# Kernel optimization log

Hardware: AMD Instinct MI355X
Metric: run time of the kernel (lower is better)

Reference implementation:

```python
import jax, jax.numpy as jnp
import numpy as np

D_MODEL = 1024
NUM_HEADS = 16
LN_EPS = 1e-5


def setup_inputs() -> dict:
    key = jax.random.key(0)
    ks = jax.random.split(key, 8)
    d = D_MODEL
    x = jax.random.normal(ks[0], (8, 1024, d), dtype=jnp.float32)
    # nn.MultiheadAttention parameters (combined in_proj, out_proj)
    in_proj_w = jax.random.normal(ks[1], (3 * d, d), dtype=jnp.float32) / np.sqrt(d)
    in_proj_b = jnp.zeros((3 * d,), dtype=jnp.float32)
    out_proj_w = jax.random.normal(ks[2], (d, d), dtype=jnp.float32) / np.sqrt(d)
    out_proj_b = jnp.zeros((d,), dtype=jnp.float32)
    ln_w = jnp.ones((d,), dtype=jnp.float32)
    ln_b = jnp.zeros((d,), dtype=jnp.float32)
    time_decay = jnp.asarray(0.1, dtype=jnp.float32)
    return {"x": x, "time_decay": time_decay, "in_proj_w": in_proj_w,
            "in_proj_b": in_proj_b, "out_proj_w": out_proj_w,
            "out_proj_b": out_proj_b, "ln_w": ln_w, "ln_b": ln_b}


def reference(x, time_decay, in_proj_w, in_proj_b, out_proj_w, out_proj_b, ln_w, ln_b):
    B, S, d = x.shape
    H = NUM_HEADS
    hd = d // H
    # vectorized time-decay bias: -|time_decay| * |i - j|  (replaces nested loop)
    idx = jnp.arange(S, dtype=jnp.float32)
    attn_bias = -jnp.abs(time_decay) * jnp.abs(idx[:, None] - idx[None, :])  # [S,S]
    # combined QKV projection
    qkv = x @ in_proj_w.T + in_proj_b  # [B,S,3d]
    q, k, v = jnp.split(qkv, 3, axis=-1)
    q = q.reshape(B, S, H, hd)
    k = k.reshape(B, S, H, hd)
    v = v.reshape(B, S, H, hd)
    scale = 1.0 / np.sqrt(hd)
    scores = jnp.einsum('bqhd,bkhd->bhqk', q, k) * scale + attn_bias  # [B,H,S,S]
    weights = jax.nn.softmax(scores, axis=-1)
    attn = jnp.einsum('bhqk,bkhd->bqhd', weights, v).reshape(B, S, d)
    attn_out = attn @ out_proj_w.T + out_proj_b
    # need_weights=True with default average_attn_weights=True -> mean over heads
    attn_weights = jnp.mean(weights, axis=1)  # [B,S,S]
    # residual + LayerNorm
    y = x + attn_out
    mu = jnp.mean(y, axis=-1, keepdims=True)
    var = jnp.mean(jnp.square(y - mu), axis=-1, keepdims=True)
    out = (y - mu) / jnp.sqrt(var + LN_EPS) * ln_w + ln_b
    return (out, attn_weights)
```

## Files before the change

kernel.cpp:

```cpp
#include <hip/hip_runtime.h>
#include <cstddef>

#define BATCH   8
#define SEQ     1024
#define DMODEL  1024
#define NHEAD   16
#define HDIM    64
#define D3      3072
#define NROWS   (BATCH * SEQ)
#define LN_EPS  1e-5f

typedef __attribute__((ext_vector_type(4))) float f32x4;
typedef __attribute__((ext_vector_type(8))) short bf16x8;

__device__ __forceinline__ float b2f(unsigned short u) {
    union { unsigned int i; float f; } v; v.i = ((unsigned int)u) << 16; return v.f;
}
__device__ __forceinline__ unsigned short f2bu(float f) {
    union { float f; unsigned int i; } v; v.f = f;
    unsigned int r = v.i + 0x7fffu + ((v.i >> 16) & 1u);
    return (unsigned short)(r >> 16);
}
__device__ __forceinline__ void gl16(const void* g, void* l) {
    __builtin_amdgcn_global_load_lds(
        (const __attribute__((address_space(1))) unsigned int*)g,
        (__attribute__((address_space(3))) unsigned int*)l, 16, 0, 0);
}

#define NG_X  1048576
#define NG_WQ 393216
#define NG_WO 131072
__global__ __launch_bounds__(256)
void cvt_bf16(const float* __restrict__ x, const float* __restrict__ wq,
              const float* __restrict__ wo,
              unsigned short* __restrict__ xb, unsigned short* __restrict__ wqb,
              unsigned short* __restrict__ wob) {
    const int gidx = blockIdx.x * 256 + threadIdx.x;
    const float* src; unsigned short* dst; size_t off;
    if (gidx < NG_X)              { src = x;  dst = xb;  off = (size_t)gidx * 8; }
    else if (gidx < NG_X + NG_WQ) { src = wq; dst = wqb; off = (size_t)(gidx - NG_X) * 8; }
    else                          { src = wo; dst = wob; off = (size_t)(gidx - NG_X - NG_WQ) * 8; }
    float4 v0 = *(const float4*)(src + off);
    float4 v1 = *(const float4*)(src + off + 4);
    uint4 pv;
    pv.x = f2bu(v0.x) | ((unsigned int)f2bu(v0.y) << 16);
    pv.y = f2bu(v0.z) | ((unsigned int)f2bu(v0.w) << 16);
    pv.z = f2bu(v1.x) | ((unsigned int)f2bu(v1.y) << 16);
    pv.w = f2bu(v1.z) | ((unsigned int)f2bu(v1.w) << 16);
    *(uint4*)(dst + off) = pv;
}

__global__ __launch_bounds__(256)
void qkv_mfma(const unsigned short* __restrict__ xb,
              const unsigned short* __restrict__ wb,
              const float* __restrict__ bias,
              unsigned short* __restrict__ qh,
              unsigned short* __restrict__ kh,
              unsigned short* __restrict__ vt) {
    __shared__ unsigned short smem[8192];
    unsigned short* As = smem;
    unsigned short* Bs = smem + 4096;

    const int t = threadIdx.x;
    const int w = t >> 6, lane = t & 63;
    const int wm = w >> 1, wn = w & 1;
    const int g = lane >> 4, c = lane & 15;
    const int m0 = blockIdx.y * 128, n0 = blockIdx.x * 128;

    const int srow = t >> 2;
    const int scol = (t & 3) * 8;
    const unsigned short* ga = xb + (size_t)(m0 + srow) * 1024 + scol;
    const unsigned short* gb = wb + (size_t)(n0 + srow) * 1024 + scol;

    f32x4 acc[4][4];
#pragma unroll
    for (int i = 0; i < 4; ++i)
#pragma unroll
        for (int j = 0; j < 4; ++j) acc[i][j] = (f32x4){0.f, 0.f, 0.f, 0.f};

    for (int k0 = 0; k0 < 1024; k0 += 32) {
        gl16(ga + k0,             As + t * 8);
        gl16(ga + 64 * 1024 + k0, As + 2048 + t * 8);
        gl16(gb + k0,             Bs + t * 8);
        gl16(gb + 64 * 1024 + k0, Bs + 2048 + t * 8);
        __syncthreads();
        bf16x8 af[4], bf[4];
#pragma unroll
        for (int i = 0; i < 4; ++i)
            af[i] = *(const bf16x8*)(As + (wm * 64 + i * 16 + c) * 32 + g * 8);
#pragma unroll
        for (int j = 0; j < 4; ++j)
            bf[j] = *(const bf16x8*)(Bs + (wn * 64 + j * 16 + c) * 32 + g * 8);
#pragma unroll
        for (int i = 0; i < 4; ++i)
#pragma unroll
            for (int j = 0; j < 4; ++j)
                acc[i][j] = __builtin_amdgcn_mfma_f32_16x16x32_bf16(af[i], bf[j], acc[i][j], 0, 0, 0);
        __syncthreads();
    }

    float bsv[4];
#pragma unroll
    for (int j = 0; j < 4; ++j) bsv[j] = bias[n0 + wn * 64 + j * 16 + c];

    unsigned short* eslice = smem + w * 2048;
    const int b_ = m0 >> 10;

    if (n0 < 2048) {
        const int ncl   = n0 + wn * 64;
        unsigned short* dst = (ncl < 1024)
            ? qh + ((size_t)(b_ * 16 + (ncl >> 6)) * 1024) * 64
            : kh + ((size_t)(b_ * 16 + ((ncl - 1024) >> 6)) * 1024) * 64;
#pragma unroll
        for (int half = 0; half < 2; ++half) {
#pragma unroll
            for (int ii = 0; ii < 2; ++ii) {
                const int i = half * 2 + ii;
#pragma unroll
                for (int j = 0; j < 4; ++j)
#pragma unroll
                    for (int r = 0; r < 4; ++r)
                        eslice[(ii * 16 + g * 4 + r) * 64 + j * 16 + c] = f2bu(acc[i][j][r] + bsv[j]);
            }
#pragma unroll
            for (int u = 0; u < 4; ++u) {
                const int mloc = u * 8 + (lane >> 3);
                const int ncol = (lane & 7) * 8;
                bf16x8 row = *(const bf16x8*)(eslice + mloc * 64 + ncol);
                const int tok = (m0 & 1023) + wm * 64 + half * 32 + mloc;
                *(bf16x8*)(dst + (size_t)tok * 64 + ncol) = row;
            }
        }
    } else {
        const int key0  = (m0 & 1023) + wm * 64;
        const int hbase = (n0 + wn * 64 - 2048) >> 6;
#pragma unroll
        for (int half = 0; half < 2; ++half) {
#pragma unroll
            for (int jj = 0; jj < 2; ++jj) {
                const int j = half * 2 + jj;
                const int nloc = jj * 16 + c;
#pragma unroll
                for (int i = 0; i < 4; ++i)
#pragma unroll
                    for (int r = 0; r < 4; ++r) {
                        const int mloc  = i * 16 + g * 4 + r;
                        const int mphys = mloc ^ ((nloc & 7) << 3);
                        eslice[nloc * 64 + mphys] = f2bu(acc[i][j][r] + bsv[j]);
                    }
            }
#pragma unroll
            for (int u = 0; u < 4; ++u) {
                const int nloc  = u * 8 + (lane >> 3);
                const int mb    = lane & 7;
                const int mphys = (mb ^ (nloc & 7)) * 8;
                bf16x8 row = *(const bf16x8*)(eslice + nloc * 64 + mphys);
                const int d = half * 32 + nloc;
                *(bf16x8*)(vt + ((size_t)((b_ * 16 + hbase) * 64 + d)) * 1024 + key0 + mb * 8) = row;
            }
        }
    }
}

__global__ __launch_bounds__(256, 2)
void attn_mfma(const unsigned short* __restrict__ qh,
               const unsigned short* __restrict__ kh,
               const unsigned short* __restrict__ vt,
               const float* __restrict__ tdp,
               unsigned short* __restrict__ attnb,
               float* __restrict__ wout) {
    const int qt = blockIdx.x;
    const int b  = blockIdx.y;
    const int t  = threadIdx.x;
    const int w  = t >> 6;
    const int lane = t & 63;
    const int g  = lane >> 4;
    const int c  = lane & 15;

    const int q0 = qt * 16;
    const float td = -fabsf(tdp[0]);

    __shared__ unsigned short P_s[16][1032];
    __shared__ float rs_s[4][16];

    float wsum[16][4];
#pragma unroll
    for (int tt = 0; tt < 16; ++tt)
#pragma unroll
        for (int r = 0; r < 4; ++r) wsum[tt][r] = 0.f;

    const int key_base = w * 256;

    for (int h = 0; h < NHEAD; ++h) {
        const unsigned short* qslab = qh + (size_t)(b * 16 + h) * 1024 * 64;
        const unsigned short* kslab = kh + (size_t)(b * 16 + h) * 1024 * 64;

        bf16x8 qa0 = *(const bf16x8*)(qslab + (size_t)(q0 + c) * 64 + g * 8);
        bf16x8 qa1 = *(const bf16x8*)(qslab + (size_t)(q0 + c) * 64 + 32 + g * 8);

        f32x4 acc[16];
#pragma unroll
        for (int tt = 0; tt < 16; ++tt) {
            const int key = key_base + tt * 16 + c;
            const unsigned short* kp = kslab + (size_t)key * 64 + g * 8;
            bf16x8 kb0 = *(const bf16x8*)(kp);
            bf16x8 kb1 = *(const bf16x8*)(kp + 32);
            f32x4 z = {0.f, 0.f, 0.f, 0.f};
            z = __builtin_amdgcn_mfma_f32_16x16x32_bf16(qa0, kb0, z, 0, 0, 0);
            z = __builtin_amdgcn_mfma_f32_16x16x32_bf16(qa1, kb1, z, 0, 0, 0);
            acc[tt] = z;
        }

        float rsum[4] = {0.f, 0.f, 0.f, 0.f};
#pragma unroll
        for (int tt = 0; tt < 16; ++tt) {
            const float kf = (float)(key_base + tt * 16 + c);
#pragma unroll
            for (int r = 0; r < 4; ++r) {
                const float qf = (float)(q0 + g * 4 + r);
                const float s = acc[tt][r] * 0.125f + td * fabsf(kf - qf);
                const float e = __expf(s);
                acc[tt][r] = e;
                rsum[r] += e;
            }
        }
#pragma unroll
        for (int r = 0; r < 4; ++r) {
            rsum[r] += __shfl_xor(rsum[r], 1, 64);
            rsum[r] += __shfl_xor(rsum[r], 2, 64);
            rsum[r] += __shfl_xor(rsum[r], 4, 64);
            rsum[r] += __shfl_xor(rsum[r], 8, 64);
        }
        if (c == 0) {
#pragma unroll
            for (int r = 0; r < 4; ++r) rs_s[w][g * 4 + r] = rsum[r];
        }
        __syncthreads();
        float invl[4];
#pragma unroll
        for (int r = 0; r < 4; ++r) {
            const int row = g * 4 + r;
            invl[r] = 1.0f / (rs_s[0][row] + rs_s[1][row] + rs_s[2][row] + rs_s[3][row]);
        }

#pragma unroll
        for (int tt = 0; tt < 16; ++tt) {
#pragma unroll
            for (int r = 0; r < 4; ++r) {
                const float wv = acc[tt][r] * invl[r];
                wsum[tt][r] += wv;
                P_s[g * 4 + r][key_base + tt * 16 + c] = f2bu(wv);
            }
        }
        __syncthreads();

        f32x4 accO = {0.f, 0.f, 0.f, 0.f};
        const unsigned short* vhp = vt + (size_t)((b * 16 + h) * 64 + w * 16 + c) * 1024;
#pragma unroll 8
        for (int ks = 0; ks < 32; ++ks) {
            bf16x8 pa = *(const bf16x8*)(&P_s[c][ks * 32 + g * 8]);
            bf16x8 vb = *(const bf16x8*)(vhp + ks * 32 + g * 8);
            accO = __builtin_amdgcn_mfma_f32_16x16x32_bf16(pa, vb, accO, 0, 0, 0);
        }
        unsigned short* op = attnb + (size_t)(b * 1024 + q0) * 1024 + h * 64 + w * 16 + c;
#pragma unroll
        for (int r = 0; r < 4; ++r)
            op[(size_t)(g * 4 + r) * 1024] = f2bu(accO[r]);
        __syncthreads();
    }

#pragma unroll
    for (int tt = 0; tt < 16; ++tt) {
#pragma unroll
        for (int r = 0; r < 4; ++r) {
            wout[(size_t)(b * 1024 + q0 + g * 4 + r) * 1024 + key_base + tt * 16 + c]
                = wsum[tt][r] * (1.0f / NHEAD);
        }
    }
}

__global__ __launch_bounds__(256)
void outproj_mfma(const unsigned short* __restrict__ ab,
                  const unsigned short* __restrict__ wob,
                  const float* __restrict__ bias,
                  const float* __restrict__ X,
                  float* __restrict__ Y) {
    __shared__ unsigned short smem[8192];
    unsigned short* As = smem;
    unsigned short* Bs = smem + 4096;

    const int t = threadIdx.x;
    const int w = t >> 6, lane = t & 63;
    const int wm = w >> 1, wn = w & 1;
    const int g = lane >> 4, c = lane & 15;
    const int m0 = blockIdx.y * 128, n0 = blockIdx.x * 128;

    const int srow = t >> 2;
    const int scol = (t & 3) * 8;
    const unsigned short* ga = ab  + (size_t)(m0 + srow) * 1024 + scol;
    const unsigned short* gb = wob + (size_t)(n0 + srow) * 1024 + scol;

    f32x4 acc[4][4];
#pragma unroll
    for (int i = 0; i < 4; ++i)
#pragma unroll
        for (int j = 0; j < 4; ++j) acc[i][j] = (f32x4){0.f, 0.f, 0.f, 0.f};

    for (int k0 = 0; k0 < 1024; k0 += 32) {
        gl16(ga + k0,             As + t * 8);
        gl16(ga + 64 * 1024 + k0, As + 2048 + t * 8);
        gl16(gb + k0,             Bs + t * 8);
        gl16(gb + 64 * 1024 + k0, Bs + 2048 + t * 8);
        __syncthreads();
        bf16x8 af[4], bf[4];
#pragma unroll
        for (int i = 0; i < 4; ++i)
            af[i] = *(const bf16x8*)(As + (wm * 64 + i * 16 + c) * 32 + g * 8);
#pragma unroll
        for (int j = 0; j < 4; ++j)
            bf[j] = *(const bf16x8*)(Bs + (wn * 64 + j * 16 + c) * 32 + g * 8);
#pragma unroll
        for (int i = 0; i < 4; ++i)
#pragma unroll
            for (int j = 0; j < 4; ++j)
                acc[i][j] = __builtin_amdgcn_mfma_f32_16x16x32_bf16(af[i], bf[j], acc[i][j], 0, 0, 0);
        __syncthreads();
    }

    float bsv[4];
#pragma unroll
    for (int j = 0; j < 4; ++j) bsv[j] = bias[n0 + wn * 64 + j * 16 + c];

#pragma unroll
    for (int i = 0; i < 4; ++i) {
#pragma unroll
        for (int r = 0; r < 4; ++r) {
            const int m = m0 + wm * 64 + i * 16 + g * 4 + r;
#pragma unroll
            for (int j = 0; j < 4; ++j) {
                const int n = n0 + wn * 64 + j * 16 + c;
                Y[(size_t)m * 1024 + n] = acc[i][j][r] + bsv[j] + X[(size_t)m * 1024 + n];
            }
        }
    }
}

__global__ __launch_bounds__(256)
void ln_kernel(const float* __restrict__ Y, const float* __restrict__ lnw,
               const float* __restrict__ lnb, float* __restrict__ out) {
    const int row = blockIdx.x, t = threadIdx.x;
    __shared__ float rs[256], rq[256];
    const float4 v = ((const float4*)(Y + (size_t)row * DMODEL))[t];
    rs[t] = v.x + v.y + v.z + v.w;
    rq[t] = v.x * v.x + v.y * v.y + v.z * v.z + v.w * v.w;
    __syncthreads();
    for (int off = 128; off > 0; off >>= 1) {
        if (t < off) { rs[t] += rs[t + off]; rq[t] += rq[t + off]; }
        __syncthreads();
    }
    const float mu   = rs[0] * (1.0f / DMODEL);
    const float var  = rq[0] * (1.0f / DMODEL) - mu * mu;
    const float rstd = rsqrtf(var + LN_EPS);
    const float4 w  = ((const float4*)lnw)[t];
    const float4 bb = ((const float4*)lnb)[t];
    float4 o;
    o.x = (v.x - mu) * rstd * w.x + bb.x;
    o.y = (v.y - mu) * rstd * w.y + bb.y;
    o.z = (v.z - mu) * rstd * w.z + bb.z;
    o.w = (v.w - mu) * rstd * w.w + bb.w;
    ((float4*)(out + (size_t)row * DMODEL))[t] = o;
}

extern "C" void kernel_launch(void* const* d_in, const int* in_sizes, int n_in,
                              void* d_out, int out_size, void* d_ws, size_t ws_size,
                              hipStream_t stream) {
    (void)in_sizes; (void)n_in; (void)out_size; (void)ws_size;
    const float* x    = (const float*)d_in[0];
    const float* td   = (const float*)d_in[1];
    const float* wqkv = (const float*)d_in[2];
    const float* bqkv = (const float*)d_in[3];
    const float* wo   = (const float*)d_in[4];
    const float* bo   = (const float*)d_in[5];
    const float* lnw  = (const float*)d_in[6];
    const float* lnb  = (const float*)d_in[7];

    float* out_ln = (float*)d_out;
    float* out_w  = (float*)d_out + (size_t)NROWS * SEQ;

    unsigned short* qh = (unsigned short*)d_ws;
    unsigned short* kh = qh + (size_t)128 * 1024 * 64;
    unsigned short* vt = kh + (size_t)128 * 1024 * 64;
    float*          y  = (float*)d_ws;

    unsigned short* attnb = (unsigned short*)d_out;
    unsigned short* wob   = (unsigned short*)d_out + (size_t)NROWS * DMODEL;
    unsigned short* xb    = (unsigned short*)out_w;
    unsigned short* wqkvb = xb + (size_t)NROWS * DMODEL;

    cvt_bf16    <<<(NG_X + NG_WQ + NG_WO) / 256, 256, 0, stream>>>(x, wqkv, wo, xb, wqkvb, wob);
    qkv_mfma    <<<dim3(D3 / 128, NROWS / 128), 256, 0, stream>>>(xb, wqkvb, bqkv, qh, kh, vt);
    attn_mfma   <<<dim3(SEQ / 16, BATCH),       256, 0, stream>>>(qh, kh, vt, td, attnb, out_w);
    outproj_mfma<<<dim3(DMODEL / 128, NROWS / 128), 256, 0, stream>>>(attnb, wob, bo, x, y);
    ln_kernel   <<<NROWS,                       256, 0, stream>>>(y, lnw, lnb, out_ln);
}
```

Baseline: 503.7 us.

## Split attention heads across grid z, defer softmax normalization, atomically accumulate weights

The attention kernel now launches two head-groups per query tile along grid z, doubling the number of blocks, and raises the launch-bounds occupancy target to 4. Exponentials are written straight into shared memory unnormalized, and the 1/rowsum scale is applied after the PV MFMA. This drops the register-held score array and one barrier per head. Because two blocks now contribute to each head-averaged weight, the output is zeroed with a memset and accumulated with atomicAdd, adding extra global traffic. The weight sums are also rebuilt from bf16-rounded probabilities, which slightly lowers precision.

Measured after the change: 511.3 us. About the same (+1.5%).

```diff
diff --git a/kernel.cpp b/kernel.cpp
--- a/kernel.cpp
+++ b/kernel.cpp
@@ -162,7 +162,7 @@
     }
 }
 
-__global__ __launch_bounds__(256, 2)
+__global__ __launch_bounds__(256, 4)
 void attn_mfma(const unsigned short* __restrict__ qh,
                const unsigned short* __restrict__ kh,
                const unsigned short* __restrict__ vt,
@@ -171,6 +171,7 @@
                float* __restrict__ wout) {
     const int qt = blockIdx.x;
     const int b  = blockIdx.y;
+    const int hg = blockIdx.z;
     const int t  = threadIdx.x;
     const int w  = t >> 6;
     const int lane = t & 63;
@@ -191,15 +192,16 @@
 
     const int key_base = w * 256;
 
-    for (int h = 0; h < NHEAD; ++h) {
+    for (int hi = 0; hi < 8; ++hi) {
+        const int h = hg * 8 + hi;
         const unsigned short* qslab = qh + (size_t)(b * 16 + h) * 1024 * 64;
         const unsigned short* kslab = kh + (size_t)(b * 16 + h) * 1024 * 64;
 
         bf16x8 qa0 = *(const bf16x8*)(qslab + (size_t)(q0 + c) * 64 + g * 8);
         bf16x8 qa1 = *(const bf16x8*)(qslab + (size_t)(q0 + c) * 64 + 32 + g * 8);
 
-        f32x4 acc[16];
-#pragma unroll
+        float rsum[4] = {0.f, 0.f, 0.f, 0.f};
+#pragma unroll 2
         for (int tt = 0; tt < 16; ++tt) {
             const int key = key_base + tt * 16 + c;
             const unsigned short* kp = kslab + (size_t)key * 64 + g * 8;
@@ -208,20 +210,13 @@
             f32x4 z = {0.f, 0.f, 0.f, 0.f};
             z = __builtin_amdgcn_mfma_f32_16x16x32_bf16(qa0, kb0, z, 0, 0, 0);
             z = __builtin_amdgcn_mfma_f32_16x16x32_bf16(qa1, kb1, z, 0, 0, 0);
-            acc[tt] = z;
-        }
-
-        float rsum[4] = {0.f, 0.f, 0.f, 0.f};
-#pragma unroll
-        for (int tt = 0; tt < 16; ++tt) {
-            const float kf = (float)(key_base + tt * 16 + c);
+            const float kf = (float)key;
 #pragma unroll
             for (int r = 0; r < 4; ++r) {
                 const float qf = (float)(q0 + g * 4 + r);
-                const float s = acc[tt][r] * 0.125f + td * fabsf(kf - qf);
-                const float e = __expf(s);
-                acc[tt][r] = e;
+                const float e = __expf(z[r] * 0.125f + td * fabsf(kf - qf));
                 rsum[r] += e;
+                P_s[g * 4 + r][key_base + tt * 16 + c] = f2bu(e);
             }
         }
 #pragma unroll
@@ -236,23 +231,13 @@
             for (int r = 0; r < 4; ++r) rs_s[w][g * 4 + r] = rsum[r];
         }
         __syncthreads();
+
         float invl[4];
 #pragma unroll
         for (int r = 0; r < 4; ++r) {
             const int row = g * 4 + r;
             invl[r] = 1.0f / (rs_s[0][row] + rs_s[1][row] + rs_s[2][row] + rs_s[3][row]);
         }
-
-#pragma unroll
-        for (int tt = 0; tt < 16; ++tt) {
-#pragma unroll
-            for (int r = 0; r < 4; ++r) {
-                const float wv = acc[tt][r] * invl[r];
-                wsum[tt][r] += wv;
-                P_s[g * 4 + r][key_base + tt * 16 + c] = f2bu(wv);
-            }
-        }
-        __syncthreads();
 
         f32x4 accO = {0.f, 0.f, 0.f, 0.f};
         const unsigned short* vhp = vt + (size_t)((b * 16 + h) * 64 + w * 16 + c) * 1024;
@@ -265,7 +250,13 @@
         unsigned short* op = attnb + (size_t)(b * 1024 + q0) * 1024 + h * 64 + w * 16 + c;
 #pragma unroll
         for (int r = 0; r < 4; ++r)
-            op[(size_t)(g * 4 + r) * 1024] = f2bu(accO[r]);
+            op[(size_t)(g * 4 + r) * 1024] = f2bu(accO[r] * invl[r]);
+
+#pragma unroll
+        for (int tt = 0; tt < 16; ++tt)
+#pragma unroll
+            for (int r = 0; r < 4; ++r)
+                wsum[tt][r] += b2f(P_s[g * 4 + r][key_base + tt * 16 + c]) * invl[r];
         __syncthreads();
     }
 
@@ -273,8 +264,8 @@
     for (int tt = 0; tt < 16; ++tt) {
 #pragma unroll
         for (int r = 0; r < 4; ++r) {
-            wout[(size_t)(b * 1024 + q0 + g * 4 + r) * 1024 + key_base + tt * 16 + c]
-                = wsum[tt][r] * (1.0f / NHEAD);
+            atomicAdd(&wout[(size_t)(b * 1024 + q0 + g * 4 + r) * 1024 + key_base + tt * 16 + c],
+                      wsum[tt][r] * (1.0f / NHEAD));
         }
     }
 }
@@ -399,7 +390,8 @@
 
     cvt_bf16    <<<(NG_X + NG_WQ + NG_WO) / 256, 256, 0, stream>>>(x, wqkv, wo, xb, wqkvb, wob);
     qkv_mfma    <<<dim3(D3 / 128, NROWS / 128), 256, 0, stream>>>(xb, wqkvb, bqkv, qh, kh, vt);
-    attn_mfma   <<<dim3(SEQ / 16, BATCH),       256, 0, stream>>>(qh, kh, vt, td, attnb, out_w);
+    hipMemsetAsync(out_w, 0, (size_t)BATCH * SEQ * SEQ * sizeof(float), stream);
+    attn_mfma   <<<dim3(SEQ / 16, BATCH, 2),    256, 0, stream>>>(qh, kh, vt, td, attnb, out_w);
     outproj_mfma<<<dim3(DMODEL / 128, NROWS / 128), 256, 0, stream>>>(attnb, wob, bo, x, y);
     ln_kernel   <<<NROWS,                       256, 0, stream>>>(y, lnw, lnb, out_ln);
 }
```
